# Kernel optimization log

Measured on AMD Instinct MI355X. Metric: run time of the kernel, lower is better.

The kernel has to match this reference:

```python
import jax, jax.numpy as jnp
import numpy as np

DN = ('NCDHW', 'OIDHW', 'NCDHW')


def conv3(x, w):
    # 3x3x3 'same' conv (submanifold conv on a dense volume == padded dense conv)
    return jax.lax.conv_general_dilated(x, w, (1, 1, 1), [(1, 1)] * 3, dimension_numbers=DN)


def conv1(x, w):
    # 1x1x1 conv
    return jax.lax.conv_general_dilated(x, w, (1, 1, 1), 'VALID', dimension_numbers=DN)


def avg_pool(x, ksz):
    s = jax.lax.reduce_window(x, 0.0, jax.lax.add, (1, 1) + ksz, (1, 1) + ksz, 'VALID')
    return s / float(np.prod(ksz))


def setup_inputs() -> dict:
    key = jax.random.key(0)
    ks = jax.random.split(key, 14)
    B, C, D, H, W = 1, 64, 48, 64, 128
    n_dense = 5  # nconvs - 1

    def he(k, shape, fan):
        return jax.random.normal(k, shape, jnp.float32) * np.sqrt(2.0 / fan).astype(np.float32)

    return {
        'fvl': jax.random.normal(ks[0], (B, C, D, H, W), jnp.float32),
        'w_a1': he(ks[1], (C, C, 3, 3, 3), 27 * C),
        'w_a2': he(ks[2], (C, C, 3, 3, 3), 27 * C),
        'w_nin': he(ks[3], (C, C, 1, 1, 1), C),
        'w1s': he(ks[4], (n_dense, C, C, 1, 1, 1), C),
        'w2s': he(ks[5], (n_dense, C, C, 1, 1, 1), C),
        'wp0': he(ks[6], (C, C, 1, 1, 1), C),
        'wp1': he(ks[7], (C, C, 1, 1, 1), C),
        'wp2': he(ks[8], (C, C, 1, 1, 1), C),
        'wp3': he(ks[9], (C, C, 1, 1, 1), C),
        'wc1': he(ks[10], (C, C, 3, 3, 3), 27 * C),
        'wc2': he(ks[11], (1, C, 3, 3, 3), 27 * 1),
        'bc': jnp.zeros((1,), jnp.float32),
    }


def reference(fvl, w_a1, w_a2, w_nin, w1s, w2s, wp0, wp1, wp2, wp3, wc1, wc2, bc):
    # --- Conv3dBlock_sparse: (conv3 -> conv3) + NIN(1x1), summed (no relu) ---
    x = conv3(conv3(fvl, w_a1), w_a2) + conv1(fvl, w_nin)
    # --- (nconvs-1) dense 1x1x1 residual blocks: relu(conv1(x) + conv2(conv1(x))) ---
    for i in range(w1s.shape[0]):
        x1 = conv1(x, w1s[i])
        x2 = conv1(x1, w2s[i])
        x = jax.nn.relu(x1 + x2)
    # --- PSP-style multi-scale pool pyramid ---
    B, C, d, h, w = x.shape
    pool_ws = [wp0, wp1, wp2, wp3]
    out_sum = x
    for i, ps in enumerate(np.linspace(1, min(d, h, w) // 2, 4, dtype=int)):
        ksz = (int(d / ps), int(h / ps), int(w / ps))
        o = avg_pool(x, ksz)
        o = conv1(o, pool_ws[i])
        o = jax.image.resize(o, (B, C, d, h, w), method='trilinear')  # align_corners=False semantics
        out_sum = out_sum + 0.25 * o
    x = jax.nn.relu(out_sum / 2.0)
    # --- classify head (eval path, up=False): conv3 -> relu -> conv3(+bias) ---
    c = conv3(jax.nn.relu(conv3(x, wc1)), wc2) + bc.reshape(1, -1, 1, 1, 1)
    return (x, jnp.squeeze(c, 1))
```

## Files before the change

### kernel.cpp

```cpp
#include <hip/hip_runtime.h>
#include <math.h>

#define DD 48
#define HH 64
#define WW 128
#define VOL (DD*HH*WW)
#define PW 130
#define PROWS (DD*HH)
#define PVOL (PROWS*PW)
#define PVBYTES ((long)PVOL*64*2)
#define GUARD 16640L
#define NC 64

typedef __attribute__((ext_vector_type(8))) short bf16x8;
typedef __attribute__((ext_vector_type(4))) float f32x4;
typedef __attribute__((ext_vector_type(4))) unsigned int u32x4v;
typedef __attribute__((ext_vector_type(2))) unsigned int u32x2v;

__device__ __forceinline__ float bflo(unsigned int u){
    union { unsigned int i; float f; } x; x.i = u<<16; return x.f; }
__device__ __forceinline__ float bfhi(unsigned int u){
    union { unsigned int i; float f; } x; x.i = u & 0xffff0000u; return x.f; }
__device__ __forceinline__ float bf2f(unsigned short u){
    union { unsigned int i; float f; } x; x.i = ((unsigned int)u)<<16; return x.f; }
__device__ __forceinline__ unsigned short f2bf(float f){
    union { float f; unsigned int i; } x; x.f = f;
    unsigned int i = x.i;
    return (unsigned short)((i + 0x7fffu + ((i>>16)&1u)) >> 16);
}

__device__ __forceinline__ void gload16(const void* g, void* l){
    __builtin_amdgcn_global_load_lds(
        (const __attribute__((address_space(1))) void*)g,
        (__attribute__((address_space(3))) void*)l, 16, 0, 0);
}

__global__ void k_prep_all(
    const float* __restrict__ w_a1, const float* __restrict__ w_a2,
    const float* __restrict__ wc1,  const float* __restrict__ wnin,
    const float* __restrict__ wc2,  const float* __restrict__ w1s,
    const float* __restrict__ w2s,  const float* __restrict__ wp1,
    const float* __restrict__ wp2,  const float* __restrict__ wp3,
    unsigned short* __restrict__ wa1t, unsigned short* __restrict__ wa2t,
    unsigned short* __restrict__ wc1t, unsigned short* __restrict__ nint,
    unsigned short* __restrict__ wt2,  unsigned short* __restrict__ Mt,
    float* __restrict__ wpt)
{
    int b = blockIdx.x, tid = threadIdx.x;
    if (b < 1296){
        int which = b/432, bb = b - which*432;
        int idx = bb*256 + tid;
        if (idx < 27*64*64){
            const float* src = which==0 ? w_a1 : (which==1 ? w_a2 : wc1);
            unsigned short* dst = which==0 ? wa1t : (which==1 ? wa2t : wc1t);
            int ci = idx & 63; int t = idx >> 6; int co = t & 63; int k = t >> 6;
            dst[idx] = f2bf(src[(co*64+ci)*27 + k]);
        }
    } else if (b < 1376){
        int idx = (b-1296)*256 + tid;
        int i = idx >> 12; int r = idx & 4095;
        int co = r >> 6; int ci = r & 63;
        const float* W1 = w1s + i*4096;
        const float* W2 = w2s + i*4096;
        float m = W1[co*64+ci];
        for (int k=0;k<64;++k) m += W2[co*64+k]*W1[k*64+ci];
        Mt[idx] = f2bf(m);
    } else if (b < 1392){
        int idx = (b-1376)*256 + tid;
        nint[idx] = f2bf(wnin[idx]);
    } else if (b < 1400){
        int idx = (b-1392)*256 + tid;
        int co = idx & 63; int row = idx >> 6;
        float v = (row < 27) ? wc2[co*27 + row] : 0.f;
        wt2[row*64 + co] = f2bf(v);
    } else {
        int bb = b - 1400;
        int which = bb/16;
        int idx = (bb - which*16)*256 + tid;
        const float* src = which==0 ? wp1 : (which==1 ? wp2 : wp3);
        int ci = idx >> 6; int co = idx & 63;
        wpt[which*4096 + idx] = src[co*64+ci];
    }
}

__global__ __launch_bounds__(256) void k_zeropad(unsigned short* __restrict__ pv0,
                                                 unsigned short* __restrict__ pv1){
    int idx = blockIdx.x*256 + threadIdx.x;
    int seg = idx >> 3, part = idx & 7;
    int vol = seg / 6144; int r2 = seg - vol*6144;
    int row = r2 >> 1; int col = (r2 & 1) ? 129 : 0;
    long boff = ((long)row*130 + col)*128 + part*16;
    u32x4v z = {0,0,0,0};
    char* base = (char*)(vol ? pv1 : pv0);
    *(u32x4v*)(base + boff) = z;
}

__global__ __launch_bounds__(256) void k_tobf16v(const float* __restrict__ src,
                                                 unsigned short* __restrict__ dst){
    __shared__ unsigned short lds[64*66];
    int tid = threadIdx.x;
    long vbase = (long)blockIdx.x*64;
    int d = (int)(vbase >> 13);
    int h = (int)((vbase >> 7) & 63);
    int w0 = (int)(vbase & 127);
    long pbase = ((long)(d*64+h)*PW + w0 + 1);
    int v = tid & 63;
    int cg = tid >> 6;
#pragma unroll
    for (int k=0;k<16;++k){
        int ci = cg*16 + k;
        lds[v*66 + ci] = f2bf(src[(long)ci*VOL + vbase + v]);
    }
    __syncthreads();
#pragma unroll
    for (int it=0; it<2; ++it){
        int chunk = it*256 + tid;
        int vv = chunk >> 3, gp = chunk & 7;
        const unsigned short* s = lds + vv*66 + gp*8;
        unsigned int w0_ = (unsigned)s[0] | ((unsigned)s[1]<<16);
        unsigned int w1_ = (unsigned)s[2] | ((unsigned)s[3]<<16);
        unsigned int w2_ = (unsigned)s[4] | ((unsigned)s[5]<<16);
        unsigned int w3_ = (unsigned)s[6] | ((unsigned)s[7]<<16);
        u32x4v q = {w0_,w1_,w2_,w3_};
        *(u32x4v*)(dst + (pbase+vv)*64 + gp*8) = q;
    }
}

template<bool AUX, bool RELU>
__global__ __launch_bounds__(256,2) void k_conv3m(
    const unsigned short* __restrict__ in, const unsigned short* __restrict__ wt,
    const unsigned short* __restrict__ aux, const unsigned short* __restrict__ auxw,
    unsigned short* __restrict__ out)
{
    __shared__ __align__(16) char sA[36864];
    __shared__ __align__(16) char sB[33280];

    const int tid  = threadIdx.x;
    const int lane = tid & 63;
    const int wave = tid >> 6;
    const int ll = lane & 15;
    const int kg = lane >> 4;
    const int bid = blockIdx.x;
    const int wid = ((bid & 7) * 192) + (bid >> 3);
    const int vbr = wid*256;
    const int d  = vbr >> 13;
    const int h0 = (vbr >> 7) & 63;
    const int my_h  = h0 + (wave >> 1);
    const int my_w0 = (wave & 1) * 64;
    const long pvb = (long)(d*64 + my_h)*PW + my_w0 + 1;

    const char* inb = (const char*)in;
    const char* wtb = (const char*)wt;

    f32x4 acc[4][4];
#pragma unroll
    for (int a=0;a<4;++a)
#pragma unroll
        for (int b=0;b<4;++b) acc[a][b] = (f32x4){0.f,0.f,0.f,0.f};

#pragma unroll
    for (int kd=0; kd<3; ++kd){
        const int dd = d + kd - 1;
        if ((unsigned)dd >= 48u) continue;
        const long rowstart = ((long)(dd*64 + h0 - 1)) * 130;
#pragma unroll
        for (int khalf=0; khalf<2; ++khalf){
            __syncthreads();
#pragma unroll
            for (int rnd=0; rnd<9; ++rnd){
                int j = rnd*4096 + tid*16;
                int q = j ^ (((j>>7)&3)<<4);
                const char* src = wtb + (long)(kd*9 + (q>>12))*8192
                                      + (long)((q>>6)&63)*128 + khalf*64 + (q&63);
                gload16(src, sA + j);
            }
#pragma unroll
            for (int rnd=0; rnd<8; ++rnd){
                int j = rnd*4096 + tid*16;
                int q = j ^ (((j>>7)&3)<<4);
                const char* src = inb + (rowstart + (q>>6))*128 + khalf*64 + (q&63);
                gload16(src, sB + j);
            }
            if (tid < 32){
                int j = 32768 + tid*16;
                int q = j ^ (((j>>7)&3)<<4);
                const char* src = inb + (rowstart + (q>>6))*128 + khalf*64 + (q&63);
                gload16(src, sB + j);
            }
            __syncthreads();
#pragma unroll
            for (int kh=0; kh<3; ++kh){
                const int hh = my_h + kh - 1;
                if ((unsigned)hh >= 64u) continue;
                const int rr = (wave>>1) + kh;
#pragma unroll
                for (int kw=0; kw<3; ++kw){
                    const int tap_rel = kh*3 + kw;
                    bf16x8 Af[4], Bf[4];
#pragma unroll
                    for (int t=0;t<4;++t){
                        int qa = tap_rel*4096 + (t*16+ll)*64 + kg*16;
                        Af[t] = *(const bf16x8*)(sA + (qa ^ (((qa>>7)&3)<<4)));
                    }
#pragma unroll
                    for (int vt=0; vt<4; ++vt){
                        int vrel = rr*130 + my_w0 + vt*16 + ll + kw;
                        int qb = vrel*64 + kg*16;
                        Bf[vt] = *(const bf16x8*)(sB + (qb ^ (((qb>>7)&3)<<4)));
                    }
#pragma unroll
                    for (int vt=0; vt<4; ++vt)
#pragma unroll
                        for (int t=0; t<4; ++t)
                            acc[t][vt] = __builtin_amdgcn_mfma_f32_16x16x32_bf16(Af[t], Bf[vt], acc[t][vt], 0,0,0);
                }
            }
        }
    }

    if (AUX){
        bf16x8 Aa[2][4], Ba[2][4];
#pragma unroll
        for (int half=0; half<2; ++half){
            const int ko = half*32 + kg*8;
#pragma unroll
            for (int t=0;t<4;++t)
                Aa[half][t] = *(const bf16x8*)(auxw + (t*16+ll)*64 + ko);
#pragma unroll
            for (int vt=0; vt<4; ++vt)
                Ba[half][vt] = *(const bf16x8*)(aux + (pvb + vt*16 + ll)*64 + ko);
        }
#pragma unroll
        for (int half=0; half<2; ++half)
#pragma unroll
            for (int vt=0; vt<4; ++vt)
#pragma unroll
                for (int t=0;t<4;++t)
                    acc[t][vt] = __builtin_amdgcn_mfma_f32_16x16x32_bf16(Aa[half][t], Ba[half][vt], acc[t][vt], 0,0,0);
    }

#pragma unroll
    for (int vt=0; vt<4; ++vt){
        unsigned short* op = out + (pvb + vt*16 + ll)*64 + kg*4;
#pragma unroll
        for (int t=0;t<4;++t){
            float r0 = acc[t][vt][0], r1 = acc[t][vt][1], r2 = acc[t][vt][2], r3 = acc[t][vt][3];
            if (RELU){ r0=fmaxf(r0,0.f); r1=fmaxf(r1,0.f); r2=fmaxf(r2,0.f); r3=fmaxf(r3,0.f); }
            unsigned int lo = (unsigned)f2bf(r0) | ((unsigned)f2bf(r1)<<16);
            unsigned int hi = (unsigned)f2bf(r2) | ((unsigned)f2bf(r3)<<16);
            u32x2v q = {lo, hi};
            *(u32x2v*)(op + t*16) = q;
        }
    }
}

__global__ __launch_bounds__(256,3) void k_chain(const unsigned short* __restrict__ in,
        const unsigned short* __restrict__ Mt, unsigned short* __restrict__ out){
    __shared__ __align__(16) char sX[4][8192];
    const int lane = threadIdx.x & 63;
    const int wave = threadIdx.x >> 6;
    const int ll = lane & 15;
    const int kg = lane >> 4;
    const long vb = (long)blockIdx.x*256 + wave*64;
    char* myL = sX[wave];

    bf16x8 B[2][4];
#pragma unroll
    for (int half=0; half<2; ++half){
        const int ko = half*32 + kg*8;
#pragma unroll
        for (int vt=0; vt<4; ++vt)
            B[half][vt] = *(const bf16x8*)(in + (vb+vt*16+ll)*64 + ko);
    }

#pragma unroll
    for (int s=0; s<5; ++s){
        const unsigned short* wt = Mt + s*4096;
        bf16x8 A[2][4];
#pragma unroll
        for (int half=0; half<2; ++half){
            const int ko = half*32 + kg*8;
#pragma unroll
            for (int t=0;t<4;++t)
                A[half][t] = *(const bf16x8*)(wt + (t*16+ll)*64 + ko);
        }
        f32x4 acc[4][4];
#pragma unroll
        for (int a=0;a<4;++a)
#pragma unroll
            for (int b=0;b<4;++b) acc[a][b] = (f32x4){0.f,0.f,0.f,0.f};
#pragma unroll
        for (int half=0; half<2; ++half)
#pragma unroll
            for (int vt=0; vt<4; ++vt)
#pragma unroll
                for (int t=0;t<4;++t)
                    acc[t][vt] = __builtin_amdgcn_mfma_f32_16x16x32_bf16(A[half][t], B[half][vt], acc[t][vt], 0,0,0);

        if (s < 4){
#pragma unroll
            for (int vt=0; vt<4; ++vt){
                const int row = vt*16 + ll;
                const int sw = (row & 7) << 4;
#pragma unroll
                for (int t=0;t<4;++t){
                    float r0 = fmaxf(acc[t][vt][0],0.f), r1 = fmaxf(acc[t][vt][1],0.f);
                    float r2 = fmaxf(acc[t][vt][2],0.f), r3 = fmaxf(acc[t][vt][3],0.f);
                    unsigned int lo = (unsigned)f2bf(r0) | ((unsigned)f2bf(r1)<<16);
                    unsigned int hi = (unsigned)f2bf(r2) | ((unsigned)f2bf(r3)<<16);
                    u32x2v q = {lo, hi};
                    int colb = kg*8 + t*32;
                    *(u32x2v*)(myL + row*128 + (colb ^ sw)) = q;
                }
            }
#pragma unroll
            for (int half=0; half<2; ++half){
#pragma unroll
                for (int vt=0; vt<4; ++vt){
                    const int row = vt*16 + ll;
                    const int sw = (row & 7) << 4;
                    int colb = half*64 + kg*16;
                    B[half][vt] = *(const bf16x8*)(myL + row*128 + (colb ^ sw));
                }
            }
        } else {
#pragma unroll
            for (int vt=0; vt<4; ++vt){
                unsigned short* op = out + (vb+vt*16+ll)*64 + kg*4;
#pragma unroll
                for (int t=0;t<4;++t){
                    float r0 = fmaxf(acc[t][vt][0],0.f), r1 = fmaxf(acc[t][vt][1],0.f);
                    float r2 = fmaxf(acc[t][vt][2],0.f), r3 = fmaxf(acc[t][vt][3],0.f);
                    unsigned int lo = (unsigned)f2bf(r0) | ((unsigned)f2bf(r1)<<16);
                    unsigned int hi = (unsigned)f2bf(r2) | ((unsigned)f2bf(r3)<<16);
                    u32x2v q = {lo, hi};
                    *(u32x2v*)(op + t*16) = q;
                }
            }
        }
    }
}

__global__ __launch_bounds__(256) void k_headt(const unsigned short* __restrict__ in,
        const unsigned short* __restrict__ wt2, unsigned short* __restrict__ t){
    const int lane = threadIdx.x & 63;
    const int wave = threadIdx.x >> 6;
    const int ll = lane & 15;
    const int kg = lane >> 4;
    const long vb = (long)blockIdx.x*256 + wave*64;

    f32x4 acc[2][4];
#pragma unroll
    for (int a=0;a<2;++a)
#pragma unroll
        for (int b=0;b<4;++b) acc[a][b] = (f32x4){0.f,0.f,0.f,0.f};

#pragma unroll
    for (int khalf=0; khalf<2; ++khalf){
        const int ko = khalf*32 + kg*8;
        bf16x8 afr[2];
#pragma unroll
        for (int tl=0;tl<2;++tl)
            afr[tl] = *(const bf16x8*)(wt2 + (tl*16+ll)*64 + ko);
#pragma unroll
        for (int vt=0; vt<4; ++vt){
            bf16x8 bfr = *(const bf16x8*)(in + (vb+vt*16+ll)*64 + ko);
#pragma unroll
            for (int tl=0;tl<2;++tl)
                acc[tl][vt] = __builtin_amdgcn_mfma_f32_16x16x32_bf16(afr[tl], bfr, acc[tl][vt], 0,0,0);
        }
    }
#pragma unroll
    for (int vt=0; vt<4; ++vt){
        long vx = vb + vt*16 + ll;
#pragma unroll
        for (int tl=0;tl<2;++tl){
#pragma unroll
            for (int r=0;r<4;++r){
                int tap = tl*16 + kg*4 + r;
                if (tap < 27) t[(long)tap*PVOL + vx] = f2bf(acc[tl][vt][r]);
            }
        }
    }
}

__global__ __launch_bounds__(256) void k_heads(const unsigned short* __restrict__ t,
        const float* __restrict__ bias, float* __restrict__ out){
    int v = blockIdx.x*256 + threadIdx.x;
    int ww = v & 127; int h = (v>>7)&63; int d = v>>13;
    long p = (long)(d*64+h)*PW + ww + 1;
    float s = bias[0];
#pragma unroll
    for (int kd=0;kd<3;++kd){
#pragma unroll
      for (int kh=0;kh<3;++kh){
#pragma unroll
        for (int kw=0;kw<3;++kw){
            const int tap = (kd*3+kh)*3+kw;
            const long dvp = (long)((kd-1)*64 + (kh-1))*PW + (kw-1);
            bool ok = ((unsigned)(d+kd-1)<48u) && ((unsigned)(h+kh-1)<64u);
            long va = ok ? (p + dvp) : p;
            float x = bf2f(t[(long)tap*PVOL + va]);
            s += ok ? x : 0.f;
        }
      }
    }
    out[v] = s;
}

__global__ __launch_bounds__(256) void k_pool3(const unsigned short* __restrict__ in,
                                               float* __restrict__ S3){
    __shared__ float sm[32*68];
    int tid = threadIdx.x;
    int cg = tid & 7, part = tid >> 3;
    int cell = blockIdx.x;
    int Z = cell >> 8, Y = (cell >> 4) & 15, X = cell & 15;
    float a[8];
#pragma unroll
    for (int j=0;j<8;++j) a[j]=0.f;
#pragma unroll
    for (int j=0;j<3;++j){
        int i = part*3 + j;
        int di = i >> 5, rem = i & 31, hi = rem >> 3, wi = rem & 7;
        long p = ((long)((3*Z+di)*64 + 4*Y+hi))*PW + 8*X+wi + 1;
        u32x4v q = *(const u32x4v*)(in + p*64 + cg*8);
#pragma unroll
        for (int e=0;e<4;++e){ a[e*2] += bflo(q[e]); a[e*2+1] += bfhi(q[e]); }
    }
#pragma unroll
    for (int j=0;j<8;++j) sm[part*68 + cg*8 + j] = a[j];
    __syncthreads();
    if (tid < 64){
        float s=0.f;
        for (int r=0;r<32;++r) s += sm[r*68 + tid];
        S3[tid*4096 + cell] = s;
    }
}

__global__ __launch_bounds__(256) void k_pool2(const float* __restrict__ S3,
                                               float* __restrict__ P2){
    int idx = blockIdx.x*256 + threadIdx.x;
    int cell = idx & 511; int c = idx >> 9;
    int z = cell >> 6, y = (cell >> 3) & 7, x = cell & 7;
    const float* b = S3 + c*4096;
    float s = 0.f;
#pragma unroll
    for (int a2=0;a2<2;++a2)
#pragma unroll
        for (int b2=0;b2<2;++b2)
#pragma unroll
            for (int e=0;e<2;++e)
                s += b[((2*z+a2)<<8) + ((2*y+b2)<<4) + (2*x+e)];
    P2[c*512 + cell] = s;
}

__global__ void k_gcm(const float* __restrict__ S3, const float* __restrict__ wp0,
                      float* __restrict__ gc){
    __shared__ float sm[4][64];
    __shared__ float sg[64];
    int tid = threadIdx.x;
    int c = tid & 63, part = tid >> 6;
    float s = 0.f;
    const float* row = S3 + c*4096 + part*1024;
    for (int i=0;i<1024;i+=4){
        f32x4 q = *(const f32x4*)(row + i);
        s += q[0]+q[1]+q[2]+q[3];
    }
    sm[part][c] = s;
    __syncthreads();
    if (tid < 64){
        sg[tid] = (sm[0][tid]+sm[1][tid]+sm[2][tid]+sm[3][tid]) * (1.0f/(float)VOL);
    }
    __syncthreads();
    if (tid < 64){
        float g=0.f;
        for (int ci=0;ci<64;++ci) g += wp0[tid*64+ci]*sg[ci];
        gc[tid] = g;
    }
}

__global__ __launch_bounds__(256) void k_pool4(const unsigned short* __restrict__ in,
                                               float* __restrict__ P4){
    __shared__ float sm[32*68];
    int tid = threadIdx.x;
    int cg = tid & 7, part = (tid >> 3) & 3, slot = tid >> 5;
    int cell = blockIdx.x*8 + slot;
    int z = cell / 800; int rem = cell - z*800; int y = rem / 25; int x = rem - y*25;
    int a2 = part >> 1, b2 = part & 1;
    float a[8];
#pragma unroll
    for (int j=0;j<8;++j) a[j]=0.f;
#pragma unroll
    for (int e=0;e<5;++e){
        long p = ((long)((2*z+a2)*64 + 2*y+b2))*PW + 5*x+e + 1;
        u32x4v q = *(const u32x4v*)(in + p*64 + cg*8);
#pragma unroll
        for (int k=0;k<4;++k){ a[k*2] += bflo(q[k]); a[k*2+1] += bfhi(q[k]); }
    }
#pragma unroll
    for (int j=0;j<8;++j) sm[(slot*4+part)*68 + cg*8 + j] = a[j];
    __syncthreads();
#pragma unroll
    for (int r=0;r<2;++r){
        int o = r*256 + tid;
        int c = o >> 3, s = o & 7;
        float v = sm[(s*4+0)*68 + c] + sm[(s*4+1)*68 + c]
                + sm[(s*4+2)*68 + c] + sm[(s*4+3)*68 + c];
        P4[(long)c*19200 + blockIdx.x*8 + s] = v;
    }
}

__global__ void k_conv1(const float* __restrict__ in, const float* __restrict__ wt,
                        float* __restrict__ out, int vol, float scale){
    int v = blockIdx.x*256 + threadIdx.x;
    if (v >= vol) return;
    float acc[64];
#pragma unroll
    for (int i=0;i<64;++i) acc[i]=0.f;
    for (int ci=0; ci<64; ++ci){
        float xv = in[ci*vol + v];
        const float* wr = wt + ci*64;
#pragma unroll
        for (int co=0; co<64; ++co) acc[co] = fmaf(wr[co], xv, acc[co]);
    }
    float* op = out + (long)v*64;
#pragma unroll
    for (int q=0;q<16;++q){
        f32x4 t = {acc[q*4]*scale, acc[q*4+1]*scale, acc[q*4+2]*scale, acc[q*4+3]*scale};
        *(f32x4*)(op + q*4) = t;
    }
}

__device__ __forceinline__ void tri_setup(int d,int h,int w,int gd,int gh,int gw,
                                          int* o, float* wt){
    float fz = (d+0.5f)*((float)gd/(float)DD) - 0.5f;
    float fy = (h+0.5f)*((float)gh/(float)HH) - 0.5f;
    float fx = (w+0.5f)*((float)gw/(float)WW) - 0.5f;
    float z0f = floorf(fz), y0f = floorf(fy), x0f = floorf(fx);
    float tz = fz - z0f, ty = fy - y0f, tx = fx - x0f;
    int z0 = (int)z0f, y0 = (int)y0f, x0 = (int)x0f;
    int z1 = z0+1, y1 = y0+1, x1 = x0+1;
    z0 = min(max(z0,0),gd-1); z1 = min(max(z1,0),gd-1);
    y0 = min(max(y0,0),gh-1); y1 = min(max(y1,0),gh-1);
    x0 = min(max(x0,0),gw-1); x1 = min(max(x1,0),gw-1);
    o[0] = (z0*gh+y0)*gw+x0; wt[0] = (1-tz)*(1-ty)*(1-tx);
    o[1] = (z0*gh+y0)*gw+x1; wt[1] = (1-tz)*(1-ty)*tx;
    o[2] = (z0*gh+y1)*gw+x0; wt[2] = (1-tz)*ty*(1-tx);
    o[3] = (z0*gh+y1)*gw+x1; wt[3] = (1-tz)*ty*tx;
    o[4] = (z1*gh+y0)*gw+x0; wt[4] = tz*(1-ty)*(1-tx);
    o[5] = (z1*gh+y0)*gw+x1; wt[5] = tz*(1-ty)*tx;
    o[6] = (z1*gh+y1)*gw+x0; wt[6] = tz*ty*(1-tx);
    o[7] = (z1*gh+y1)*gw+x1; wt[7] = tz*ty*tx;
}

__global__ __launch_bounds__(256) void k_combine(
        const unsigned short* __restrict__ xc, const float* __restrict__ gc,
        const float* __restrict__ p2, const float* __restrict__ p3,
        const float* __restrict__ p4, float* __restrict__ xout,
        unsigned short* __restrict__ xv){
    int tid = threadIdx.x;
    const int bid = blockIdx.x;
    const int wid = ((bid & 7) * 384) + (bid >> 3);
    const int half = tid >> 7;
    long v = (long)wid*128 + (tid & 127);
    int w = v & 127; int h = (v>>7)&63; int d = v>>13;
    long p = (long)(d*64+h)*PW + w + 1;
    int o2[8], o3[8], o4[8];
    float w2_[8], w3_[8], w4_[8];
    tri_setup(d,h,w, 8,8,8,    o2, w2_);
    tri_setup(d,h,w, 16,16,16, o3, w3_);
    tri_setup(d,h,w, 24,32,25, o4, w4_);

    float res[32];
#pragma unroll
    for (int j=0;j<32;++j) res[j] = gc[half*32+j];
#pragma unroll
    for (int t=0;t<8;++t){
        const float* b2 = p2 + (long)o2[t]*64 + half*32;
#pragma unroll
        for (int q=0;q<8;++q){
            f32x4 x4 = *(const f32x4*)(b2 + q*4);
            res[q*4+0] = fmaf(w2_[t], x4[0], res[q*4+0]);
            res[q*4+1] = fmaf(w2_[t], x4[1], res[q*4+1]);
            res[q*4+2] = fmaf(w2_[t], x4[2], res[q*4+2]);
            res[q*4+3] = fmaf(w2_[t], x4[3], res[q*4+3]);
        }
    }
#pragma unroll
    for (int t=0;t<8;++t){
        const float* b3 = p3 + (long)o3[t]*64 + half*32;
#pragma unroll
        for (int q=0;q<8;++q){
            f32x4 x4 = *(const f32x4*)(b3 + q*4);
            res[q*4+0] = fmaf(w3_[t], x4[0], res[q*4+0]);
            res[q*4+1] = fmaf(w3_[t], x4[1], res[q*4+1]);
            res[q*4+2] = fmaf(w3_[t], x4[2], res[q*4+2]);
            res[q*4+3] = fmaf(w3_[t], x4[3], res[q*4+3]);
        }
    }
#pragma unroll
    for (int t=0;t<8;++t){
        const float* b4 = p4 + (long)o4[t]*64 + half*32;
#pragma unroll
        for (int q=0;q<8;++q){
            f32x4 x4 = *(const f32x4*)(b4 + q*4);
            res[q*4+0] = fmaf(w4_[t], x4[0], res[q*4+0]);
            res[q*4+1] = fmaf(w4_[t], x4[1], res[q*4+1]);
            res[q*4+2] = fmaf(w4_[t], x4[2], res[q*4+2]);
            res[q*4+3] = fmaf(w4_[t], x4[3], res[q*4+3]);
        }
    }
    const u32x4v* xq = (const u32x4v*)(xc + p*64 + half*32);
#pragma unroll
    for (int q=0;q<4;++q){
        u32x4v qv = xq[q];
        unsigned int pk[4];
#pragma unroll
        for (int e=0;e<4;++e){
            int j = q*8 + e*2;
            float r0 = fmaxf((bflo(qv[e]) + 0.25f*res[j])*0.5f, 0.f);
            float r1 = fmaxf((bfhi(qv[e]) + 0.25f*res[j+1])*0.5f, 0.f);
            __builtin_nontemporal_store(r0, &xout[(long)(half*32+j)*VOL + v]);
            __builtin_nontemporal_store(r1, &xout[(long)(half*32+j+1)*VOL + v]);
            pk[e] = (unsigned)f2bf(r0) | ((unsigned)f2bf(r1)<<16);
        }
        u32x4v pq = {pk[0],pk[1],pk[2],pk[3]};
        *(u32x4v*)(xv + p*64 + half*32 + q*8) = pq;
    }
}

constexpr long RPV = GUARD + PVBYTES + GUARD;
constexpr long OFF_PV0R = 0;
constexpr long OFF_PV1R = RPV;
constexpr long OFF_WA1 = 2*RPV;
constexpr long OFF_WA2 = OFF_WA1 + 221184;
constexpr long OFF_WC1 = OFF_WA2 + 221184;
constexpr long OFF_NIN = OFF_WC1 + 221184;
constexpr long OFF_MT  = OFF_NIN + 8192;
constexpr long OFF_WT2 = OFF_MT + 40960;
constexpr long OFF_WPT = OFF_WT2 + 4096;
constexpr long OFF_GC  = OFF_WPT + 49152;
constexpr long OFF_P2  = OFF_GC + 256;
constexpr long OFF_P2C = OFF_P2 + 131072;
constexpr long OFF_S3  = OFF_P2C + 131072;
constexpr long OFF_P3C = OFF_S3 + 1048576;
constexpr long OFF_P4  = OFF_P3C + 1048576;
constexpr long OFF_P4C = OFF_P4 + 4915200;

extern "C" void kernel_launch(void* const* d_in, const int* in_sizes, int n_in,
                              void* d_out, int out_size, void* d_ws, size_t ws_size,
                              hipStream_t stream) {
    const float* fvl  = (const float*)d_in[0];
    const float* w_a1 = (const float*)d_in[1];
    const float* w_a2 = (const float*)d_in[2];
    const float* wnin = (const float*)d_in[3];
    const float* w1s  = (const float*)d_in[4];
    const float* w2s  = (const float*)d_in[5];
    const float* wp0  = (const float*)d_in[6];
    const float* wp1  = (const float*)d_in[7];
    const float* wp2  = (const float*)d_in[8];
    const float* wp3  = (const float*)d_in[9];
    const float* wc1  = (const float*)d_in[10];
    const float* wc2  = (const float*)d_in[11];
    const float* bc   = (const float*)d_in[12];

    char* ws = (char*)d_ws;
    unsigned short* PV0  = (unsigned short*)(ws + OFF_PV0R + GUARD);
    unsigned short* PV1  = (unsigned short*)(ws + OFF_PV1R + GUARD);
    unsigned short* wa1t = (unsigned short*)(ws + OFF_WA1);
    unsigned short* wa2t = (unsigned short*)(ws + OFF_WA2);
    unsigned short* wc1t = (unsigned short*)(ws + OFF_WC1);
    unsigned short* nint = (unsigned short*)(ws + OFF_NIN);
    unsigned short* Mt   = (unsigned short*)(ws + OFF_MT);
    unsigned short* wt2  = (unsigned short*)(ws + OFF_WT2);
    float* wpt  = (float*)(ws + OFF_WPT);
    float* gc   = (float*)(ws + OFF_GC);
    float* p2   = (float*)(ws + OFF_P2);
    float* p2c  = (float*)(ws + OFF_P2C);
    float* S3   = (float*)(ws + OFF_S3);
    float* p3c  = (float*)(ws + OFF_P3C);
    float* p4   = (float*)(ws + OFF_P4);
    float* p4c  = (float*)(ws + OFF_P4C);

    float* Xout = (float*)d_out;
    float* Cout = Xout + (long)NC*VOL;
    unsigned short* Tbuf = (unsigned short*)PV0;

    const int GBR = VOL/256;
    const int GBP = PVOL/256;

    k_zeropad<<<384,256,0,stream>>>(PV0, PV1);

    k_prep_all<<<1448,256,0,stream>>>(w_a1, w_a2, wc1, wnin, wc2, w1s, w2s,
                                      wp1, wp2, wp3,
                                      wa1t, wa2t, wc1t, nint, wt2, Mt, wpt);
    k_tobf16v<<<VOL/64,256,0,stream>>>(fvl, PV0);

    k_conv3m<false,false><<<GBR,256,0,stream>>>(PV0, wa1t, nullptr, nullptr, PV1);
    k_conv3m<true,false><<<GBR,256,0,stream>>>(PV1, wa2t, PV0, nint, PV0);

    k_chain<<<GBP,256,0,stream>>>(PV0, Mt, PV1);

    k_pool3<<<4096,256,0,stream>>>(PV1, S3);
    k_gcm<<<1,256,0,stream>>>(S3, wp0, gc);
    k_pool2<<<128,256,0,stream>>>(S3, p2);
    k_pool4<<<2400,256,0,stream>>>(PV1, p4);
    k_conv1<<<2,256,0,stream>>>(p2, wpt + 0*4096, p2c, 512,   1.0f/768.0f);
    k_conv1<<<16,256,0,stream>>>(S3, wpt + 1*4096, p3c, 4096, 1.0f/96.0f);
    k_conv1<<<75,256,0,stream>>>(p4, wpt + 2*4096, p4c, 19200, 1.0f/20.0f);

    k_combine<<<3072,256,0,stream>>>(PV1, gc, p2c, p3c, p4c, Xout, PV0);

    k_conv3m<false,true><<<GBR,256,0,stream>>>(PV0, wc1t, nullptr, nullptr, PV1);
    k_headt<<<GBP,256,0,stream>>>(PV1, wt2, Tbuf);
    k_heads<<<GBR,256,0,stream>>>(Tbuf, bc, Cout);
}
```

Baseline: 600.3 us.

## Fuse head conv3+relu with per-tap 1x1 projection; reshape combine grid

Adds a fused kernel that runs the classify-head 3x3x3 conv with ReLU and, in the same block, projects the result through the 27-tap weight matrix from LDS. This removes the write and re-read of the 64-channel intermediate volume and one launch. The tap buffer now lives in PV1, and the tap gather gains a w-boundary check, since the fused kernel writes only interior columns and no longer fills the pad columns. k_combine now gives each thread both channel halves over 256 voxels, which halves the block count and doubles per-thread work.

```diff
diff --git a/kernel.cpp b/kernel.cpp
--- a/kernel.cpp
+++ b/kernel.cpp
@@ -254,6 +254,150 @@
     }
 }
 
+__global__ __launch_bounds__(256,2) void k_conv3h(
+    const unsigned short* __restrict__ in, const unsigned short* __restrict__ wt,
+    const unsigned short* __restrict__ wt2, unsigned short* __restrict__ t)
+{
+    __shared__ __align__(16) char sA[36864];
+    __shared__ __align__(16) char sB[33280];
+
+    const int tid  = threadIdx.x;
+    const int lane = tid & 63;
+    const int wave = tid >> 6;
+    const int ll = lane & 15;
+    const int kg = lane >> 4;
+    const int bid = blockIdx.x;
+    const int wid = ((bid & 7) * 192) + (bid >> 3);
+    const int vbr = wid*256;
+    const int d  = vbr >> 13;
+    const int h0 = (vbr >> 7) & 63;
+    const int my_h  = h0 + (wave >> 1);
+    const int my_w0 = (wave & 1) * 64;
+    const long pvb = (long)(d*64 + my_h)*PW + my_w0 + 1;
+
+    const char* inb = (const char*)in;
+    const char* wtb = (const char*)wt;
+
+    f32x4 acc[4][4];
+#pragma unroll
+    for (int a=0;a<4;++a)
+#pragma unroll
+        for (int b=0;b<4;++b) acc[a][b] = (f32x4){0.f,0.f,0.f,0.f};
+
+#pragma unroll
+    for (int kd=0; kd<3; ++kd){
+        const int dd = d + kd - 1;
+        if ((unsigned)dd >= 48u) continue;
+        const long rowstart = ((long)(dd*64 + h0 - 1)) * 130;
+#pragma unroll
+        for (int khalf=0; khalf<2; ++khalf){
+            __syncthreads();
+#pragma unroll
+            for (int rnd=0; rnd<9; ++rnd){
+                int j = rnd*4096 + tid*16;
+                int q = j ^ (((j>>7)&3)<<4);
+                const char* src = wtb + (long)(kd*9 + (q>>12))*8192
+                                      + (long)((q>>6)&63)*128 + khalf*64 + (q&63);
+                gload16(src, sA + j);
+            }
+#pragma unroll
+            for (int rnd=0; rnd<8; ++rnd){
+                int j = rnd*4096 + tid*16;
+                int q = j ^ (((j>>7)&3)<<4);
+                const char* src = inb + (rowstart + (q>>6))*128 + khalf*64 + (q&63);
+                gload16(src, sB + j);
+            }
+            if (tid < 32){
+                int j = 32768 + tid*16;
+                int q = j ^ (((j>>7)&3)<<4);
+                const char* src = inb + (rowstart + (q>>6))*128 + khalf*64 + (q&63);
+                gload16(src, sB + j);
+            }
+            __syncthreads();
+#pragma unroll
+            for (int kh=0; kh<3; ++kh){
+                const int hh = my_h + kh - 1;
+                if ((unsigned)hh >= 64u) continue;
+                const int rr = (wave>>1) + kh;
+#pragma unroll
+                for (int kw=0; kw<3; ++kw){
+                    const int tap_rel = kh*3 + kw;
+                    bf16x8 Af[4], Bf[4];
+#pragma unroll
+                    for (int tt=0;tt<4;++tt){
+                        int qa = tap_rel*4096 + (tt*16+ll)*64 + kg*16;
+                        Af[tt] = *(const bf16x8*)(sA + (qa ^ (((qa>>7)&3)<<4)));
+                    }
+#pragma unroll
+                    for (int vt=0; vt<4; ++vt){
+                        int vrel = rr*130 + my_w0 + vt*16 + ll + kw;
+                        int qb = vrel*64 + kg*16;
+                        Bf[vt] = *(const bf16x8*)(sB + (qb ^ (((qb>>7)&3)<<4)));
+                    }
+#pragma unroll
+                    for (int vt=0; vt<4; ++vt)
+#pragma unroll
+                        for (int tt=0; tt<4; ++tt)
+                            acc[tt][vt] = __builtin_amdgcn_mfma_f32_16x16x32_bf16(Af[tt], Bf[vt], acc[tt][vt], 0,0,0);
+                }
+            }
+        }
+    }
+
+    __syncthreads();
+    char* myL = sA + wave*8192;
+#pragma unroll
+    for (int vt=0; vt<4; ++vt){
+        const int row = vt*16 + ll;
+        const int sw = (row & 7) << 4;
+#pragma unroll
+        for (int tt=0;tt<4;++tt){
+            float r0 = fmaxf(acc[tt][vt][0],0.f), r1 = fmaxf(acc[tt][vt][1],0.f);
+            float r2 = fmaxf(acc[tt][vt][2],0.f), r3 = fmaxf(acc[tt][vt][3],0.f);
+            unsigned int lo = (unsigned)f2bf(r0) | ((unsigned)f2bf(r1)<<16);
+            unsigned int hi = (unsigned)f2bf(r2) | ((unsigned)f2bf(r3)<<16);
+            u32x2v q = {lo, hi};
+            int colb = kg*8 + tt*32;
+            *(u32x2v*)(myL + row*128 + (colb ^ sw)) = q;
+        }
+    }
+    f32x4 acc2[2][4];
+#pragma unroll
+    for (int a=0;a<2;++a)
+#pragma unroll
+        for (int b=0;b<4;++b) acc2[a][b] = (f32x4){0.f,0.f,0.f,0.f};
+#pragma unroll
+    for (int half=0; half<2; ++half){
+        const int ko = half*32 + kg*8;
+        bf16x8 afr[2];
+#pragma unroll
+        for (int tl=0;tl<2;++tl)
+            afr[tl] = *(const bf16x8*)(wt2 + (tl*16+ll)*64 + ko);
+#pragma unroll
+        for (int vt=0; vt<4; ++vt){
+            const int row = vt*16 + ll;
+            const int sw = (row & 7) << 4;
+            int colb = half*64 + kg*16;
+            bf16x8 bfr = *(const bf16x8*)(myL + row*128 + (colb ^ sw));
+#pragma unroll
+            for (int tl=0;tl<2;++tl)
+                acc2[tl][vt] = __builtin_amdgcn_mfma_f32_16x16x32_bf16(afr[tl], bfr, acc2[tl][vt], 0,0,0);
+        }
+    }
+#pragma unroll
+    for (int vt=0; vt<4; ++vt){
+        long vx = pvb + vt*16 + ll;
+#pragma unroll
+        for (int tl=0;tl<2;++tl){
+#pragma unroll
+            for (int r=0;r<4;++r){
+                int tap = tl*16 + kg*4 + r;
+                if (tap < 27) t[(long)tap*PVOL + vx] = f2bf(acc2[tl][vt][r]);
+            }
+        }
+    }
+}
+
 __global__ __launch_bounds__(256,3) void k_chain(const unsigned short* __restrict__ in,
         const unsigned short* __restrict__ Mt, unsigned short* __restrict__ out){
     __shared__ __align__(16) char sX[4][8192];
@@ -341,49 +485,6 @@
     }
 }
 
-__global__ __launch_bounds__(256) void k_headt(const unsigned short* __restrict__ in,
-        const unsigned short* __restrict__ wt2, unsigned short* __restrict__ t){
-    const int lane = threadIdx.x & 63;
-    const int wave = threadIdx.x >> 6;
-    const int ll = lane & 15;
-    const int kg = lane >> 4;
-    const long vb = (long)blockIdx.x*256 + wave*64;
-
-    f32x4 acc[2][4];
-#pragma unroll
-    for (int a=0;a<2;++a)
-#pragma unroll
-        for (int b=0;b<4;++b) acc[a][b] = (f32x4){0.f,0.f,0.f,0.f};
-
-#pragma unroll
-    for (int khalf=0; khalf<2; ++khalf){
-        const int ko = khalf*32 + kg*8;
-        bf16x8 afr[2];
-#pragma unroll
-        for (int tl=0;tl<2;++tl)
-            afr[tl] = *(const bf16x8*)(wt2 + (tl*16+ll)*64 + ko);
-#pragma unroll
-        for (int vt=0; vt<4; ++vt){
-            bf16x8 bfr = *(const bf16x8*)(in + (vb+vt*16+ll)*64 + ko);
-#pragma unroll
-            for (int tl=0;tl<2;++tl)
-                acc[tl][vt] = __builtin_amdgcn_mfma_f32_16x16x32_bf16(afr[tl], bfr, acc[tl][vt], 0,0,0);
-        }
-    }
-#pragma unroll
-    for (int vt=0; vt<4; ++vt){
-        long vx = vb + vt*16 + ll;
-#pragma unroll
-        for (int tl=0;tl<2;++tl){
-#pragma unroll
-            for (int r=0;r<4;++r){
-                int tap = tl*16 + kg*4 + r;
-                if (tap < 27) t[(long)tap*PVOL + vx] = f2bf(acc[tl][vt][r]);
-            }
-        }
-    }
-}
-
 __global__ __launch_bounds__(256) void k_heads(const unsigned short* __restrict__ t,
         const float* __restrict__ bias, float* __restrict__ out){
     int v = blockIdx.x*256 + threadIdx.x;
@@ -398,7 +499,8 @@
         for (int kw=0;kw<3;++kw){
             const int tap = (kd*3+kh)*3+kw;
             const long dvp = (long)((kd-1)*64 + (kh-1))*PW + (kw-1);
-            bool ok = ((unsigned)(d+kd-1)<48u) && ((unsigned)(h+kh-1)<64u);
+            bool ok = ((unsigned)(d+kd-1)<48u) && ((unsigned)(h+kh-1)<64u)
+                   && ((unsigned)(ww+kw-1)<128u);
             long va = ok ? (p + dvp) : p;
             float x = bf2f(t[(long)tap*PVOL + va]);
             s += ok ? x : 0.f;
@@ -560,9 +662,8 @@
         unsigned short* __restrict__ xv){
     int tid = threadIdx.x;
     const int bid = blockIdx.x;
-    const int wid = ((bid & 7) * 384) + (bid >> 3);
-    const int half = tid >> 7;
-    long v = (long)wid*128 + (tid & 127);
+    const int wid = ((bid & 7) * 192) + (bid >> 3);
+    long v = (long)wid*256 + tid;
     int w = v & 127; int h = (v>>7)&63; int d = v>>13;
     long p = (long)(d*64+h)*PW + w + 1;
     int o2[8], o3[8], o4[8];
@@ -570,62 +671,64 @@
     tri_setup(d,h,w, 8,8,8,    o2, w2_);
     tri_setup(d,h,w, 16,16,16, o3, w3_);
     tri_setup(d,h,w, 24,32,25, o4, w4_);
-
-    float res[32];
-#pragma unroll
-    for (int j=0;j<32;++j) res[j] = gc[half*32+j];
-#pragma unroll
-    for (int t=0;t<8;++t){
-        const float* b2 = p2 + (long)o2[t]*64 + half*32;
-#pragma unroll
-        for (int q=0;q<8;++q){
-            f32x4 x4 = *(const f32x4*)(b2 + q*4);
-            res[q*4+0] = fmaf(w2_[t], x4[0], res[q*4+0]);
-            res[q*4+1] = fmaf(w2_[t], x4[1], res[q*4+1]);
-            res[q*4+2] = fmaf(w2_[t], x4[2], res[q*4+2]);
-            res[q*4+3] = fmaf(w2_[t], x4[3], res[q*4+3]);
-        }
-    }
-#pragma unroll
-    for (int t=0;t<8;++t){
-        const float* b3 = p3 + (long)o3[t]*64 + half*32;
-#pragma unroll
-        for (int q=0;q<8;++q){
-            f32x4 x4 = *(const f32x4*)(b3 + q*4);
-            res[q*4+0] = fmaf(w3_[t], x4[0], res[q*4+0]);
-            res[q*4+1] = fmaf(w3_[t], x4[1], res[q*4+1]);
-            res[q*4+2] = fmaf(w3_[t], x4[2], res[q*4+2]);
-            res[q*4+3] = fmaf(w3_[t], x4[3], res[q*4+3]);
-        }
-    }
-#pragma unroll
-    for (int t=0;t<8;++t){
-        const float* b4 = p4 + (long)o4[t]*64 + half*32;
-#pragma unroll
-        for (int q=0;q<8;++q){
-            f32x4 x4 = *(const f32x4*)(b4 + q*4);
-            res[q*4+0] = fmaf(w4_[t], x4[0], res[q*4+0]);
-            res[q*4+1] = fmaf(w4_[t], x4[1], res[q*4+1]);
-            res[q*4+2] = fmaf(w4_[t], x4[2], res[q*4+2]);
-            res[q*4+3] = fmaf(w4_[t], x4[3], res[q*4+3]);
-        }
-    }
-    const u32x4v* xq = (const u32x4v*)(xc + p*64 + half*32);
-#pragma unroll
-    for (int q=0;q<4;++q){
-        u32x4v qv = xq[q];
-        unsigned int pk[4];
-#pragma unroll
-        for (int e=0;e<4;++e){
-            int j = q*8 + e*2;
-            float r0 = fmaxf((bflo(qv[e]) + 0.25f*res[j])*0.5f, 0.f);
-            float r1 = fmaxf((bfhi(qv[e]) + 0.25f*res[j+1])*0.5f, 0.f);
-            __builtin_nontemporal_store(r0, &xout[(long)(half*32+j)*VOL + v]);
-            __builtin_nontemporal_store(r1, &xout[(long)(half*32+j+1)*VOL + v]);
-            pk[e] = (unsigned)f2bf(r0) | ((unsigned)f2bf(r1)<<16);
-        }
-        u32x4v pq = {pk[0],pk[1],pk[2],pk[3]};
-        *(u32x4v*)(xv + p*64 + half*32 + q*8) = pq;
+#pragma unroll
+    for (int half=0; half<2; ++half){
+        float res[32];
+#pragma unroll
+        for (int j=0;j<32;++j) res[j] = gc[half*32+j];
+#pragma unroll
+        for (int t=0;t<8;++t){
+            const float* b2 = p2 + (long)o2[t]*64 + half*32;
+#pragma unroll
+            for (int q=0;q<8;++q){
+                f32x4 x4 = *(const f32x4*)(b2 + q*4);
+                res[q*4+0] = fmaf(w2_[t], x4[0], res[q*4+0]);
+                res[q*4+1] = fmaf(w2_[t], x4[1], res[q*4+1]);
+                res[q*4+2] = fmaf(w2_[t], x4[2], res[q*4+2]);
+                res[q*4+3] = fmaf(w2_[t], x4[3], res[q*4+3]);
+            }
+        }
+#pragma unroll
+        for (int t=0;t<8;++t){
+            const float* b3 = p3 + (long)o3[t]*64 + half*32;
+#pragma unroll
+            for (int q=0;q<8;++q){
+                f32x4 x4 = *(const f32x4*)(b3 + q*4);
+                res[q*4+0] = fmaf(w3_[t], x4[0], res[q*4+0]);
+                res[q*4+1] = fmaf(w3_[t], x4[1], res[q*4+1]);
+                res[q*4+2] = fmaf(w3_[t], x4[2], res[q*4+2]);
+                res[q*4+3] = fmaf(w3_[t], x4[3], res[q*4+3]);
+            }
+        }
+#pragma unroll
+        for (int t=0;t<8;++t){
+            const float* b4 = p4 + (long)o4[t]*64 + half*32;
+#pragma unroll
+            for (int q=0;q<8;++q){
+                f32x4 x4 = *(const f32x4*)(b4 + q*4);
+                res[q*4+0] = fmaf(w4_[t], x4[0], res[q*4+0]);
+                res[q*4+1] = fmaf(w4_[t], x4[1], res[q*4+1]);
+                res[q*4+2] = fmaf(w4_[t], x4[2], res[q*4+2]);
+                res[q*4+3] = fmaf(w4_[t], x4[3], res[q*4+3]);
+            }
+        }
+        const u32x4v* xq = (const u32x4v*)(xc + p*64 + half*32);
+#pragma unroll
+        for (int q=0;q<4;++q){
+            u32x4v qv = xq[q];
+            unsigned int pk[4];
+#pragma unroll
+            for (int e=0;e<4;++e){
+                int j = q*8 + e*2;
+                float r0 = fmaxf((bflo(qv[e]) + 0.25f*res[j])*0.5f, 0.f);
+                float r1 = fmaxf((bfhi(qv[e]) + 0.25f*res[j+1])*0.5f, 0.f);
+                __builtin_nontemporal_store(r0, &xout[(long)(half*32+j)*VOL + v]);
+                __builtin_nontemporal_store(r1, &xout[(long)(half*32+j+1)*VOL + v]);
+                pk[e] = (unsigned)f2bf(r0) | ((unsigned)f2bf(r1)<<16);
+            }
+            u32x4v pq = {pk[0],pk[1],pk[2],pk[3]};
+            *(u32x4v*)(xv + p*64 + half*32 + q*8) = pq;
+        }
     }
 }
 
@@ -684,7 +787,7 @@
 
     float* Xout = (float*)d_out;
     float* Cout = Xout + (long)NC*VOL;
-    unsigned short* Tbuf = (unsigned short*)PV0;
+    unsigned short* Tbuf = PV1;
 
     const int GBR = VOL/256;
     const int GBP = PVOL/256;
@@ -709,9 +812,8 @@
     k_conv1<<<16,256,0,stream>>>(S3, wpt + 1*4096, p3c, 4096, 1.0f/96.0f);
     k_conv1<<<75,256,0,stream>>>(p4, wpt + 2*4096, p4c, 19200, 1.0f/20.0f);
 
-    k_combine<<<3072,256,0,stream>>>(PV1, gc, p2c, p3c, p4c, Xout, PV0);
-
-    k_conv3m<false,true><<<GBR,256,0,stream>>>(PV0, wc1t, nullptr, nullptr, PV1);
-    k_headt<<<GBP,256,0,stream>>>(PV1, wt2, Tbuf);
+    k_combine<<<GBR,256,0,stream>>>(PV1, gc, p2c, p3c, p4c, Xout, PV0);
+
+    k_conv3h<<<GBR,256,0,stream>>>(PV0, wc1t, wt2, Tbuf);
     k_heads<<<GBR,256,0,stream>>>(Tbuf, bc, Cout);
 }
```

After: 580.9 us. 3.2% less time.
